# Performance work log

Measured on AMD Instinct MI355X. Metric: run time of the kernel, lower is better.

Reference implementation:

```python
import jax, jax.numpy as jnp
import numpy as np

LN_EPS = 1e-5
FD_EPS = 1e-3   # cfg.fd_eps
MAX_ITER = 2    # cfg.max_iter; early-exit on tol is a host-side .item() check in torch, omitted for jit (fixed iterations)


def _block(w1, b1, w2, b2, g, beta, x):
    # pre-LN MLP residual block: x + W2 @ gelu(W1 @ LN(x))
    mu = jnp.mean(x, axis=-1, keepdims=True)
    var = jnp.var(x, axis=-1, keepdims=True)
    xn = (x - mu) * jax.lax.rsqrt(var + LN_EPS) * g + beta
    h = jax.nn.gelu(xn @ w1 + b1)
    return x + h @ w2 + b2

# apply block_l to state_l for all l at once: (L,B,T,C) -> (L,B,T,C)
_vblock = jax.vmap(_block, in_axes=(0, 0, 0, 0, 0, 0, 0))


def _scan_solve(As, bs):
    # solve x_l = A_l * x_{l-1} + b_l with x_0 = b_0 (A_0 unused), O(log L)
    def combine(e1, e2):
        A1, c1 = e1
        A2, c2 = e2
        return A2 * A1, A2 * c1 + c2
    _, xs = jax.lax.associative_scan(combine, (As, bs), axis=0)
    return xs


def setup_inputs() -> dict:
    key = jax.random.key(0)
    ks = jax.random.split(key, 3)
    L, B, T, C, F = 12, 2, 512, 768, 3072
    return {
        "x0": jax.random.normal(ks[0], (B, T, C), jnp.float32),
        "w1": jax.random.normal(ks[1], (L, C, F), jnp.float32) * 0.02,
        "b1": jnp.zeros((L, F), jnp.float32),
        "w2": jax.random.normal(ks[2], (L, F, C), jnp.float32) * 0.02,
        "b2": jnp.zeros((L, C), jnp.float32),
        "g": jnp.ones((L, C), jnp.float32),
        "beta": jnp.zeros((L, C), jnp.float32),
    }


def reference(x0, w1, b1, w2, b2, g, beta):
    L = w1.shape[0]
    # picard warmstart: states[l+1] = block_l(x0) (computed under torch.no_grad)
    warm = jax.lax.stop_gradient(
        _vblock(w1, b1, w2, b2, g, beta, jnp.broadcast_to(x0, (L,) + x0.shape)))
    states = jnp.concatenate([x0[None], warm], axis=0)  # (L+1, B, T, C)
    key = jax.random.key(42)
    for it in range(MAX_ITER):
        # residuals r_l = block_l(x_l) - x_{l+1}
        outs = _vblock(w1, b1, w2, b2, g, beta, states[:-1])
        res = outs - states[1:]
        # quasi-DEER FD diagonal Jacobian (Rademacher probe, under no_grad)
        sg = jax.lax.stop_gradient(states[:-1])
        v = jnp.sign(jax.random.normal(jax.random.fold_in(key, it), sg.shape, jnp.float32))
        op = _vblock(w1, b1, w2, b2, g, beta, sg + FD_EPS * v)
        om = _vblock(w1, b1, w2, b2, g, beta, sg - FD_EPS * v)
        diag_J = jax.lax.stop_gradient((op - om) / (2.0 * FD_EPS) * v)
        # damping k=0 for quasi-deer -> A_l = diag_J_l, b_l = r_l
        delta = _scan_solve(diag_J, res)  # (L, B, T, C)
        states = states.at[1:].add(delta)
    return states[-1]
```

## Files before the change

### kernel.cpp

```cpp
#include <hip/hip_runtime.h>
#include <hip/hip_bf16.h>
#include <stdint.h>


typedef __bf16 bf16;
typedef __bf16 bf16x8 __attribute__((ext_vector_type(8)));
typedef float f32x4 __attribute__((ext_vector_type(4)));

#define LAY_A   1572864
#define LAY_W   2359296
#define LAY_Z   6291456
#define LAY_S   786432

#define GLDS16(gp, lp) __builtin_amdgcn_global_load_lds(                      \
    (const __attribute__((address_space(1))) void*)(gp),                      \
    (__attribute__((address_space(3))) void*)(lp), 16, 0, 0)

#define WAITVM(N) asm volatile("s_waitcnt vmcnt(%0)" :: "n"(N) : "memory")
#define CFENCE()  asm volatile("" ::: "memory")

#define TF_ROT(x0, x1, n) { x0 += x1; x1 = (x1 << n) | (x1 >> (32 - n)); x1 ^= x0; }
__host__ __device__ __forceinline__ void threefry2x32(
    uint32_t k1, uint32_t k2, uint32_t c0, uint32_t c1, uint32_t& o0, uint32_t& o1)
{
  const uint32_t ks2 = k1 ^ k2 ^ 0x1BD11BDAu;
  uint32_t x0 = c0 + k1, x1 = c1 + k2;
  TF_ROT(x0,x1,13) TF_ROT(x0,x1,15) TF_ROT(x0,x1,26) TF_ROT(x0,x1,6)
  x0 += k2;  x1 += ks2 + 1u;
  TF_ROT(x0,x1,17) TF_ROT(x0,x1,29) TF_ROT(x0,x1,16) TF_ROT(x0,x1,24)
  x0 += ks2; x1 += k1 + 2u;
  TF_ROT(x0,x1,13) TF_ROT(x0,x1,15) TF_ROT(x0,x1,26) TF_ROT(x0,x1,6)
  x0 += k1;  x1 += k2 + 3u;
  TF_ROT(x0,x1,17) TF_ROT(x0,x1,29) TF_ROT(x0,x1,16) TF_ROT(x0,x1,24)
  x0 += k2;  x1 += ks2 + 4u;
  TF_ROT(x0,x1,13) TF_ROT(x0,x1,15) TF_ROT(x0,x1,26) TF_ROT(x0,x1,6)
  x0 += ks2; x1 += k1 + 5u;
  o0 = x0; o1 = x1;
}

__global__ __launch_bounds__(256) void transpose_kernel(
    const float* __restrict__ w, bf16* __restrict__ wt, int R, int Cc)
{
  __shared__ float tile[32][33];
  const int l = blockIdx.z;
  const float* wp = w + (size_t)l * R * Cc;
  bf16* wtp = wt + (size_t)l * R * Cc;
  const int c0 = blockIdx.x * 32;
  const int r0 = blockIdx.y * 32;
  const int tx = threadIdx.x & 31, ty = threadIdx.x >> 5;
  #pragma unroll
  for (int q = 0; q < 4; ++q)
    tile[ty + q * 8][tx] = wp[(size_t)(r0 + ty + q * 8) * Cc + c0 + tx];
  __syncthreads();
  const int orow = threadIdx.x >> 4;
  const int oc   = (threadIdx.x & 15) * 2;
  #pragma unroll
  for (int q = 0; q < 2; ++q) {
    const int r = orow + q * 16;
    const unsigned short lo = __builtin_bit_cast(unsigned short,
                                                 (bf16)tile[oc][r]);
    const unsigned short hi = __builtin_bit_cast(unsigned short,
                                                 (bf16)tile[oc + 1][r]);
    *(unsigned int*)&wtp[(size_t)(c0 + r) * R + r0 + oc] =
        (unsigned int)lo | ((unsigned int)hi << 16);
  }
}

__device__ __forceinline__ void gelu2(float z, float& h, float& dg)
{
  const float z2 = z * z;
  const float u = 0.7978845608028654f * (z + 0.044715f * z2 * z);
  const float e = __expf(2.0f * u);
  const float t = 1.0f - 2.0f / (e + 1.0f);
  h = 0.5f * z * (1.f + t);
  dg = 0.5f * (1.f + t) +
       0.5f * z * (1.f - t * t) * 0.7978845608028654f * (1.f + 0.134145f * z2);
}

template <int MODE>
__global__ __launch_bounds__(256, 2) void gemm_dbuf(
    const bf16* __restrict__ Abase, const bf16* __restrict__ Bbase,
    bf16* __restrict__ zh_out, float* __restrict__ states,
    float* __restrict__ resA, const bf16* __restrict__ vbuf,
    const float* __restrict__ bias1, const float* __restrict__ b2,
    const float* __restrict__ x0, int Mt)
{
  constexpr int LDAB  = (MODE <= 1) ? 768 : 3072;
  constexpr int NKT   = (MODE <= 1) ? 12 : 48;
  constexpr int NTN   = (MODE <= 1) ? 24 : 6;
  constexpr int ACH   = 16;
  constexpr int BCH   = 16;
  constexpr int NCH   = (ACH + BCH) / 4;
  constexpr int ABYTES = 16384;
  constexpr int TILE  = ABYTES + BCH * 1024;
  constexpr size_t LSA = (MODE <= 1) ? LAY_A : LAY_Z;

  __shared__ __align__(16) char lds[2][TILE];

  const int tid  = threadIdx.x;
  const int lane = tid & 63;
  const int wid  = tid >> 6;
  const int wr   = wid >> 1;
  const int wc   = wid & 1;
  const int r16  = lane & 15;
  const int hi   = lane >> 4;

  const int nwg = gridDim.x;
  const int bid = blockIdx.x;
  const int swz = (bid & 7) * (nwg >> 3) + (bid >> 3);
  const int per_l = Mt * NTN;
  const int l   = swz / per_l;
  const int rr_ = swz - l * per_l;
  const int mt  = rr_ / NTN;
  const int nt  = rr_ - mt * NTN;
  const int m0  = mt * 128, n0 = nt * 128;

  const bf16* A = Abase + (size_t)l * LSA   + (size_t)m0 * LDAB;
  const bf16* B = Bbase + (size_t)l * LAY_W + (size_t)n0 * LDAB;

  const int rsub = lane >> 3;
  const int c8   = (lane & 7) ^ rsub;
  auto STAGE = [&](char* dst, int kt) {
    #pragma unroll
    for (int j = 0; j < NCH; ++j) {
      const int chunk = j * 4 + wid;
      if (chunk < ACH) {
        const int row = chunk * 8 + rsub;
        GLDS16(A + (size_t)row * LDAB + kt + c8 * 8, dst + chunk * 1024);
      } else {
        const int row = (chunk - ACH) * 8 + rsub;
        GLDS16(B + (size_t)row * LDAB + kt + c8 * 8,
               dst + ABYTES + (chunk - ACH) * 1024);
      }
    }
  };

  f32x4 acc[4][4] = {};

  auto COMPUTE = [&](const char* buf) {
    const char* As = buf;
    const char* Bs = buf + ABYTES;
    const int xw = (r16 & 7) << 4;
    #pragma unroll
    for (int kk = 0; kk < 2; ++kk) {
      const int cb = kk * 64;
      bf16x8 bfrag[4];
      #pragma unroll
      for (int ni = 0; ni < 4; ++ni) {
        const int rn = wc * 64 + ni * 16 + r16;
        bfrag[ni] = *(const bf16x8*)(Bs + rn * 128 + ((cb + hi * 16) ^ xw));
      }
      bf16x8 afrag[4];
      #pragma unroll
      for (int q = 0; q < 4; ++q) {
        const int rm = wr * 64 + q * 16 + r16;
        afrag[q] = *(const bf16x8*)(As + rm * 128 + ((cb + hi * 16) ^ xw));
      }
      #pragma unroll
      for (int q = 0; q < 4; ++q)
        #pragma unroll
        for (int ni = 0; ni < 4; ++ni)
          acc[q][ni] = __builtin_amdgcn_mfma_f32_16x16x32_bf16(
              afrag[q], bfrag[ni], acc[q][ni], 0, 0, 0);
    }
  };

  STAGE(lds[0], 0);
  STAGE(lds[1], 64);
  WAITVM(NCH);
  __builtin_amdgcn_s_barrier();
  CFENCE();
  COMPUTE(lds[0]);
  #pragma unroll 1
  for (int t = 1; t < NKT; ++t) {
    CFENCE();
    __builtin_amdgcn_s_barrier();
    CFENCE();
    if (t + 1 < NKT) {
      STAGE(lds[(t + 1) & 1], (t + 1) * 64);
      WAITVM(NCH);
    } else {
      WAITVM(0);
    }
    __builtin_amdgcn_s_barrier();
    CFENCE();
    COMPUTE(lds[t & 1]);
  }

  #pragma unroll
  for (int mi = 0; mi < 4; ++mi) {
    const int row0 = m0 + wr * 64 + mi * 16 + hi * 4;
    #pragma unroll
    for (int ni = 0; ni < 4; ++ni) {
      const int col = n0 + wc * 64 + ni * 16 + r16;
      if (MODE == 0) {
        bf16* Cp = zh_out + (size_t)l * LAY_Z;
        const float bias = bias1[l * 3072 + col];
        #pragma unroll
        for (int r = 0; r < 4; ++r) {
          float h, dg;
          gelu2(acc[mi][ni][r] + bias, h, dg);
          Cp[(size_t)(row0 + r) * 3072 + col] = (bf16)h;
        }
      } else if (MODE == 1) {
        bf16* Cp = zh_out + (size_t)l * LAY_Z;
        const float bias = bias1[l * 3072 + col];
        #pragma unroll
        for (int p = 0; p < 2; ++p) {
          float h, dg;
          gelu2(acc[mi][ni][2 * p] + bias, h, dg);
          Cp[(size_t)(row0 + 2 * p) * 3072 + col] = (bf16)h;
          Cp[(size_t)(row0 + 2 * p + 1) * 3072 + col] =
              (bf16)(dg * acc[mi][ni][2 * p + 1]);
        }
      } else if (MODE == 2) {
        float* Sp = states + (size_t)(l + 1) * LAY_S;
        const float bb = b2[l * 768 + col];
        #pragma unroll
        for (int r = 0; r < 4; ++r)
          Sp[(size_t)(row0 + r) * 768 + col] =
              acc[mi][ni][r] + bb + x0[(size_t)(row0 + r) * 768 + col];
      } else {
        float* Rp = resA + (size_t)l * LAY_A;
        const float bb = b2[l * 768 + col];
        #pragma unroll
        for (int p = 0; p < 2; ++p) {
          const int tok = (row0 >> 1) + p;
          Rp[(size_t)tok * 768 + col] = acc[mi][ni][2 * p] + bb
              + states[(size_t)l * LAY_S + (size_t)tok * 768 + col]
              - states[(size_t)(l + 1) * LAY_S + (size_t)tok * 768 + col];
          const float vv = (float)vbuf[(size_t)l * LAY_S +
                                       (size_t)tok * 768 + col];
          Rp[LAY_S + (size_t)tok * 768 + col] =
              1.0f + acc[mi][ni][2 * p + 1] * vv;
        }
      }
    }
  }
}

__global__ __launch_bounds__(256) void ln_warm_kernel(
    const float* __restrict__ x0, const float* __restrict__ g,
    const float* __restrict__ beta, bf16* __restrict__ a_buf,
    float* __restrict__ st0)
{
  const int row = blockIdx.x * 4 + (threadIdx.x >> 6);
  const int lane = threadIdx.x & 63;
  const float* x = x0 + (size_t)row * 768;
  float* s0 = st0 + (size_t)row * 768;
  float xl[12];
  float s1 = 0.f, s2 = 0.f;
  #pragma unroll
  for (int j = 0; j < 12; ++j) {
    float t = x[lane + 64 * j];
    xl[j] = t; s1 += t; s2 += t * t;
    s0[lane + 64 * j] = t;
  }
  #pragma unroll
  for (int off = 1; off < 64; off <<= 1) {
    s1 += __shfl_xor(s1, off);
    s2 += __shfl_xor(s2, off);
  }
  const float mu = s1 * (1.f / 768.f);
  const float var = s2 * (1.f / 768.f) - mu * mu;
  const float rstd = rsqrtf(var + 1e-5f);
  float xh[12];
  #pragma unroll
  for (int j = 0; j < 12; ++j) xh[j] = (xl[j] - mu) * rstd;
  for (int l = 0; l < 12; ++l) {
    const float* gp = g + l * 768;
    const float* bp = beta + l * 768;
    bf16* ap = a_buf + (size_t)l * LAY_A + (size_t)row * 768;
    #pragma unroll
    for (int j = 0; j < 12; ++j) {
      const int c = lane + 64 * j;
      ap[c] = (bf16)(xh[j] * gp[c] + bp[c]);
    }
  }
}

__global__ __launch_bounds__(256) void ln_iter_kernel(
    const float* __restrict__ states, bf16* __restrict__ vbuf,
    const float* __restrict__ g, const float* __restrict__ beta,
    bf16* __restrict__ a_buf, uint32_t k1, uint32_t k2)
{
  const int gr = blockIdx.x * 4 + (threadIdx.x >> 6);
  const int l = gr >> 10;
  const int row = gr & 1023;
  const int lane = threadIdx.x & 63;
  const float* x = states + (size_t)l * LAY_S + (size_t)row * 768;
  bf16* vp = vbuf + (size_t)gr * 768;
  float xl[12], vl[12];
  float s1 = 0.f, s2 = 0.f, sv = 0.f, sxv = 0.f;
  #pragma unroll
  for (int j = 0; j < 12; ++j) {
    const int c = lane + 64 * j;
    const float t = x[c];
    uint32_t o0, o1;
    threefry2x32(k1, k2, 0u, (uint32_t)gr * 768u + (uint32_t)c, o0, o1);
    const float u = ((o0 ^ o1) & 0x80000000u) ? 1.0f : -1.0f;
    vp[c] = (bf16)u;
    xl[j] = t; vl[j] = u;
    s1 += t; s2 += t * t; sv += u; sxv += t * u;
  }
  #pragma unroll
  for (int off = 1; off < 64; off <<= 1) {
    s1 += __shfl_xor(s1, off); s2 += __shfl_xor(s2, off);
    sv += __shfl_xor(sv, off); sxv += __shfl_xor(sxv, off);
  }
  const float mu = s1 * (1.f / 768.f);
  const float var = s2 * (1.f / 768.f) - mu * mu;
  const float rstd = rsqrtf(var + 1e-5f);
  const float mv = sv * (1.f / 768.f);
  const float mhv = rstd * (sxv * (1.f / 768.f) - mu * mv);
  const float* gp = g + l * 768;
  const float* bp = beta + l * 768;
  bf16* ap = a_buf + (size_t)l * LAY_A + (size_t)(2 * row) * 768;
  bf16* dp = ap + 768;
  #pragma unroll
  for (int j = 0; j < 12; ++j) {
    const int c = lane + 64 * j;
    const float xh = (xl[j] - mu) * rstd;
    ap[c] = (bf16)(xh * gp[c] + bp[c]);
    dp[c] = (bf16)(rstd * ((vl[j] - mv) - xh * mhv) * gp[c]);
  }
}

__global__ __launch_bounds__(256) void scan_kernel(
    const float* __restrict__ resA, float* __restrict__ states,
    float* __restrict__ dout)
{
  const size_t i = (size_t)blockIdx.x * 256 + threadIdx.x;
  float run = resA[i];
  float v = states[LAY_S + i] + run;
  states[LAY_S + i] = v;
  #pragma unroll
  for (int l = 1; l < 12; ++l) {
    const float b  = resA[(size_t)l * LAY_A + i];
    const float Aa = resA[(size_t)l * LAY_A + LAY_S + i];
    run = b + Aa * run;
    v = states[(size_t)(l + 1) * LAY_S + i] + run;
    states[(size_t)(l + 1) * LAY_S + i] = v;
  }
  dout[i] = v;
}

extern "C" void kernel_launch(void* const* d_in, const int* in_sizes, int n_in,
                              void* d_out, int out_size, void* d_ws, size_t ws_size,
                              hipStream_t stream)
{
  const float* x0   = (const float*)d_in[0];
  const float* w1   = (const float*)d_in[1];
  const float* b1   = (const float*)d_in[2];
  const float* w2   = (const float*)d_in[3];
  const float* b2   = (const float*)d_in[4];
  const float* g    = (const float*)d_in[5];
  const float* beta = (const float*)d_in[6];

  char* ws = (char*)d_ws;
  size_t off = 0;
  auto alloc = [&](size_t bytes) -> void* {
    void* p = ws + off;
    off += (bytes + 255) & ~(size_t)255;
    return p;
  };
  bf16*  w1t    = (bf16*)alloc(2ULL * 12 * LAY_W);
  bf16*  w2t    = (bf16*)alloc(2ULL * 12 * LAY_W);
  float* states = (float*)alloc(4ULL * 13 * LAY_S);
  bf16*  a_buf  = (bf16*)alloc(2ULL * 12 * LAY_A);
  bf16*  zh     = (bf16*)alloc(2ULL * 12 * LAY_Z);
  float* resA   = (float*)alloc(4ULL * 12 * LAY_A);
  bf16*  vbuf   = (bf16*)alloc(2ULL * 12 * LAY_S);

  transpose_kernel<<<dim3(96, 24, 12), 256, 0, stream>>>(w1, w1t, 768, 3072);
  transpose_kernel<<<dim3(24, 96, 12), 256, 0, stream>>>(w2, w2t, 3072, 768);

  ln_warm_kernel<<<256, 256, 0, stream>>>(x0, g, beta, a_buf, states);
  gemm_dbuf<0><<<2304, 256, 0, stream>>>(a_buf, w1t, zh, states, resA, vbuf,
                                         b1, b2, x0, 8);
  gemm_dbuf<2><<<576, 256, 0, stream>>>(zh, w2t, nullptr, states, resA, vbuf,
                                        b1, b2, x0, 8);

  for (int it = 0; it < 2; ++it) {
    uint32_t k1, k2;
    threefry2x32(0u, 42u, 0u, (uint32_t)it, k1, k2);
    ln_iter_kernel<<<3072, 256, 0, stream>>>(states, vbuf, g, beta, a_buf,
                                             k1, k2);
    gemm_dbuf<1><<<4608, 256, 0, stream>>>(a_buf, w1t, zh, states, resA, vbuf,
                                           b1, b2, x0, 16);
    gemm_dbuf<3><<<1152, 256, 0, stream>>>(zh, w2t, nullptr, states, resA, vbuf,
                                           b1, b2, x0, 16);
    scan_kernel<<<3072, 256, 0, stream>>>(resA, states, (float*)d_out);
  }
}
```

Baseline: 992.9 us.

## Fuse first-iteration scan with second-iteration LayerNorm/probe prep; shrink final scan

Merges the scan update of iteration one with the LayerNorm, Rademacher probe generation and tangent computation of iteration two into one row-wise kernel. Each wave now walks all 12 layers for one row while keeping the updated state in registers, so the separate ln_iter launch and its state re-read go away. The final scan no longer writes back every intermediate state and only emits the output. In exchange the fused kernel launches just 256 blocks with a serial 12-layer loop per row, which lowers parallelism and could leave the GPU underused.

```diff
diff --git a/kernel.cpp b/kernel.cpp
--- a/kernel.cpp
+++ b/kernel.cpp
@@ -326,23 +326,84 @@
   }
 }
 
-__global__ __launch_bounds__(256) void scan_kernel(
+__global__ __launch_bounds__(256) void scan_ln_kernel(
     const float* __restrict__ resA, float* __restrict__ states,
+    const float* __restrict__ g, const float* __restrict__ beta,
+    bf16* __restrict__ a_buf, bf16* __restrict__ vbuf,
+    uint32_t k1, uint32_t k2)
+{
+  const int row = blockIdx.x * 4 + (threadIdx.x >> 6);
+  const int lane = threadIdx.x & 63;
+  float cur[12], rn[12];
+  #pragma unroll
+  for (int j = 0; j < 12; ++j)
+    cur[j] = states[(size_t)row * 768 + lane + 64 * j];
+
+  #pragma unroll 1
+  for (int l = 0; l < 12; ++l) {
+    float vl[12];
+    float s1 = 0.f, s2 = 0.f, sv = 0.f, sxv = 0.f;
+    #pragma unroll
+    for (int j = 0; j < 12; ++j) {
+      const int c = lane + 64 * j;
+      uint32_t o0, o1;
+      threefry2x32(k1, k2, 0u,
+                   (uint32_t)(l * 1024 + row) * 768u + (uint32_t)c, o0, o1);
+      const float u = ((o0 ^ o1) & 0x80000000u) ? 1.0f : -1.0f;
+      vbuf[(size_t)l * LAY_S + (size_t)row * 768 + c] = (bf16)u;
+      vl[j] = u;
+      const float t = cur[j];
+      s1 += t; s2 += t * t; sv += u; sxv += t * u;
+    }
+    #pragma unroll
+    for (int off = 1; off < 64; off <<= 1) {
+      s1 += __shfl_xor(s1, off); s2 += __shfl_xor(s2, off);
+      sv += __shfl_xor(sv, off); sxv += __shfl_xor(sxv, off);
+    }
+    const float mu = s1 * (1.f / 768.f);
+    const float var = s2 * (1.f / 768.f) - mu * mu;
+    const float rstd = rsqrtf(var + 1e-5f);
+    const float mv = sv * (1.f / 768.f);
+    const float mhv = rstd * (sxv * (1.f / 768.f) - mu * mv);
+    const float* gp = g + l * 768;
+    const float* bp = beta + l * 768;
+    bf16* ap = a_buf + (size_t)l * LAY_A + (size_t)(2 * row) * 768;
+    bf16* dp = ap + 768;
+    #pragma unroll
+    for (int j = 0; j < 12; ++j) {
+      const int c = lane + 64 * j;
+      const float xh = (cur[j] - mu) * rstd;
+      ap[c] = (bf16)(xh * gp[c] + bp[c]);
+      dp[c] = (bf16)(rstd * ((vl[j] - mv) - xh * mhv) * gp[c]);
+    }
+    const float* Rp = resA + (size_t)l * LAY_A + (size_t)row * 768;
+    float* Sp = states + (size_t)(l + 1) * LAY_S + (size_t)row * 768;
+    #pragma unroll
+    for (int j = 0; j < 12; ++j) {
+      const int c = lane + 64 * j;
+      const float b  = Rp[c];
+      const float Aa = Rp[LAY_S + c];
+      rn[j] = (l == 0) ? b : (b + Aa * rn[j]);
+      const float v = Sp[c] + rn[j];
+      Sp[c] = v;
+      cur[j] = v;
+    }
+  }
+}
+
+__global__ __launch_bounds__(256) void scan_final_kernel(
+    const float* __restrict__ resA, const float* __restrict__ states,
     float* __restrict__ dout)
 {
   const size_t i = (size_t)blockIdx.x * 256 + threadIdx.x;
   float run = resA[i];
-  float v = states[LAY_S + i] + run;
-  states[LAY_S + i] = v;
   #pragma unroll
   for (int l = 1; l < 12; ++l) {
     const float b  = resA[(size_t)l * LAY_A + i];
     const float Aa = resA[(size_t)l * LAY_A + LAY_S + i];
     run = b + Aa * run;
-    v = states[(size_t)(l + 1) * LAY_S + i] + run;
-    states[(size_t)(l + 1) * LAY_S + i] = v;
-  }
-  dout[i] = v;
+  }
+  dout[i] = states[12ULL * LAY_S + i] + run;
 }
 
 extern "C" void kernel_launch(void* const* d_in, const int* in_sizes, int n_in,
@@ -381,15 +442,22 @@
   gemm_dbuf<2><<<576, 256, 0, stream>>>(zh, w2t, nullptr, states, resA, vbuf,
                                         b1, b2, x0, 8);
 
-  for (int it = 0; it < 2; ++it) {
-    uint32_t k1, k2;
-    threefry2x32(0u, 42u, 0u, (uint32_t)it, k1, k2);
-    ln_iter_kernel<<<3072, 256, 0, stream>>>(states, vbuf, g, beta, a_buf,
-                                             k1, k2);
-    gemm_dbuf<1><<<4608, 256, 0, stream>>>(a_buf, w1t, zh, states, resA, vbuf,
-                                           b1, b2, x0, 16);
-    gemm_dbuf<3><<<1152, 256, 0, stream>>>(zh, w2t, nullptr, states, resA, vbuf,
-                                           b1, b2, x0, 16);
-    scan_kernel<<<3072, 256, 0, stream>>>(resA, states, (float*)d_out);
-  }
-}
+  uint32_t k1a, k2a, k1b, k2b;
+  threefry2x32(0u, 42u, 0u, 0u, k1a, k2a);
+  threefry2x32(0u, 42u, 0u, 1u, k1b, k2b);
+
+  ln_iter_kernel<<<3072, 256, 0, stream>>>(states, vbuf, g, beta, a_buf,
+                                           k1a, k2a);
+  gemm_dbuf<1><<<4608, 256, 0, stream>>>(a_buf, w1t, zh, states, resA, vbuf,
+                                         b1, b2, x0, 16);
+  gemm_dbuf<3><<<1152, 256, 0, stream>>>(zh, w2t, nullptr, states, resA, vbuf,
+                                         b1, b2, x0, 16);
+  scan_ln_kernel<<<256, 256, 0, stream>>>(resA, states, g, beta, a_buf, vbuf,
+                                          k1b, k2b);
+
+  gemm_dbuf<1><<<4608, 256, 0, stream>>>(a_buf, w1t, zh, states, resA, vbuf,
+                                         b1, b2, x0, 16);
+  gemm_dbuf<3><<<1152, 256, 0, stream>>>(zh, w2t, nullptr, states, resA, vbuf,
+                                         b1, b2, x0, 16);
+  scan_final_kernel<<<3072, 256, 0, stream>>>(resA, states, (float*)d_out);
+}
```

New measurement: 1.050 ms. 1.06x slower.
